# Kernel tuning notes

Measured on AMD Instinct MI355X. Metric: run time of the kernel, lower is better.

Reference implementation:

```python
import jax, jax.numpy as jnp
import numpy as np

N = 50000        # atoms
E = 1600000      # edges (precomputed radius graph)
H = 128          # hidden_channels
F = 64           # num_filters
G = 50           # num_gaussians
L = 3            # num_interactions
NG = 256         # graphs in batch
MAXZ = 100       # atomic-number vocabulary
CUTOFF = 10.0


def ssp(x):
    # ShiftedSoftplus
    return jax.nn.softplus(x) - jnp.log(2.0).astype(x.dtype)


def setup_inputs() -> dict:
    key = jax.random.key(0)
    ks = jax.random.split(key, 20)
    s = 0.1
    inp = {
        "z": jax.random.randint(ks[0], (N,), 0, MAXZ),
        "pos": jax.random.uniform(ks[1], (N, 3), dtype=jnp.float32) * 5.0,
        "batch": jnp.sort(jax.random.randint(ks[2], (N,), 0, NG)),
        "edge_index": jax.random.randint(ks[3], (2, E), 0, N),
        "emb": jax.random.normal(ks[4], (MAXZ, H), dtype=jnp.float32),
        # interaction-block params, stacked over L layers
        "mw1": jax.random.normal(ks[5], (L, G, F), dtype=jnp.float32) * s,
        "mb1": jnp.zeros((L, F), dtype=jnp.float32),
        "mw2": jax.random.normal(ks[6], (L, F, F), dtype=jnp.float32) * s,
        "mb2": jnp.zeros((L, F), dtype=jnp.float32),
        "l1w": jax.random.normal(ks[7], (L, H, F), dtype=jnp.float32) * s,  # no bias
        "l2w": jax.random.normal(ks[8], (L, F, H), dtype=jnp.float32) * s,
        "l2b": jnp.zeros((L, H), dtype=jnp.float32),
        "lw": jax.random.normal(ks[9], (L, H, H), dtype=jnp.float32) * s,
        "lb": jnp.zeros((L, H), dtype=jnp.float32),
        # output MLP
        "ow1": jax.random.normal(ks[10], (H, H // 2), dtype=jnp.float32) * s,
        "ob1": jnp.zeros((H // 2,), dtype=jnp.float32),
        "ow2": jax.random.normal(ks[11], (H // 2, 1), dtype=jnp.float32) * s,
        "ob2": jnp.zeros((1,), dtype=jnp.float32),
    }
    return inp


def reference(z, pos, batch, edge_index, emb, mw1, mb1, mw2, mb2,
              l1w, l2w, l2b, lw, lb, ow1, ob1, ow2, ob2):
    src = edge_index[0]  # j (message source)
    dst = edge_index[1]  # i (message target)

    h = emb[z]                                   # [N,H]

    # edge distances + Gaussian smearing
    d = jnp.linalg.norm(pos[src] - pos[dst], axis=-1)          # [E]
    offset = jnp.linspace(0.0, CUTOFF, G, dtype=jnp.float32)   # [G]
    coeff = -0.5 / (offset[1] - offset[0]) ** 2
    edge_attr = jnp.exp(coeff * (d[:, None] - offset) ** 2)    # [E,G]

    # cosine cutoff
    C = 0.5 * (jnp.cos(d * jnp.pi / CUTOFF) + 1.0)             # [E]

    for i in range(L):
        # per-edge filter MLP
        W = ssp(edge_attr @ mw1[i] + mb1[i]) @ mw2[i] + mb2[i]  # [E,F]
        W = W * C[:, None]
        xj = (h @ l1w[i])[src]                                  # gather [E,F]
        msg = xj * W                                            # [E,F]
        agg = jax.ops.segment_sum(msg, dst, num_segments=N)     # [N,F]
        x = agg @ l2w[i] + l2b[i]                               # [N,H]
        x = ssp(x)
        x = x @ lw[i] + lb[i]
        h = h + x                                               # residual

    # output network + per-graph sum readout
    h = ssp(h @ ow1 + ob1)
    h = h @ ow2 + ob2                                           # [N,1]
    out = jax.ops.segment_sum(h, batch, num_segments=NG)        # [NG,1]
    return out.squeeze(1)                                       # [NG]
```

## Files before the change

kernel.cpp:

```cpp
#include <hip/hip_runtime.h>


typedef short bf16x8 __attribute__((ext_vector_type(8)));
typedef unsigned short ushort8 __attribute__((ext_vector_type(8)));
typedef float floatx4 __attribute__((ext_vector_type(4)));

#define HCH 128
#define FCH 64
#define GCH 50
#define LN  3
#define TBL 4096
#define CAP2 12288
#define CHUNK 4096
#define DMAX 8.6603f

#define MFMA(a, b, c) __builtin_amdgcn_mfma_f32_16x16x32_bf16((a), (b), (c), 0, 0, 0)

__device__ __forceinline__ unsigned short f2bf(float x) {
    unsigned int u = __float_as_uint(x);
    unsigned int r = (u + 0x7FFFu + ((u >> 16) & 1u)) >> 16;
    return (unsigned short)r;
}

__device__ __forceinline__ unsigned pk2bf(float lo, float hi) {
    unsigned ulo = __float_as_uint(lo) + 0x8000u;
    unsigned uhi = __float_as_uint(hi) + 0x8000u;
    return __builtin_amdgcn_perm(uhi, ulo, 0x07060302u);
}

__device__ __forceinline__ float bf2f(unsigned short u) {
    return __uint_as_float((unsigned)u << 16);
}

__device__ __forceinline__ float sspf(float x) {
    float t = __expf(-fabsf(x));
    float l = __logf(1.f + t);
    return fmaxf(x, 0.f) + l - 0.69314718056f;
}

__device__ __forceinline__ void fill_frag(const float* __restrict__ src,
                                          short* __restrict__ dst,
                                          int K, int F, int Ksrc,
                                          int tid, int nthr)
{
    int kc = K >> 5;
    int total = (F >> 4) * kc * 512;
    for (int i = tid; i < total; i += nthr) {
        int j = i & 7;
        int lane = (i >> 3) & 63;
        int rest = i >> 9;
        int kk = rest % kc;
        int nt = rest / kc;
        int k = kk * 32 + ((lane >> 4) << 3) + j;
        int f = nt * 16 + (lane & 15);
        float v = (k < Ksrc) ? src[k * F + f] : 0.f;
        dst[i] = (short)f2bf(v);
    }
}

__global__ void k_prep(const float* __restrict__ l1w, const float* __restrict__ l2w,
                       const float* __restrict__ lw,  const float* __restrict__ ow1,
                       short* __restrict__ l1wp, short* __restrict__ l2wp,
                       short* __restrict__ lwp,  short* __restrict__ ow1p)
{
    int tid = blockIdx.x * blockDim.x + threadIdx.x;
    int nthr = gridDim.x * blockDim.x;
    for (int l = 0; l < LN; l++) {
        fill_frag(l1w + l * HCH * FCH, l1wp + l * 8192, 128, 64, 128, tid, nthr);
        fill_frag(l2w + l * FCH * HCH, l2wp + l * 8192, 64, 128, 64, tid, nthr);
        fill_frag(lw  + l * HCH * HCH, lwp  + l * 16384, 128, 128, 128, tid, nthr);
    }
    fill_frag(ow1, ow1p, 128, 64, 128, tid, nthr);
}

__global__ __launch_bounds__(64) void k_wtab(
    const float* __restrict__ mw1, const float* __restrict__ mb1,
    const float* __restrict__ mw2, const float* __restrict__ mb2,
    unsigned short* __restrict__ Wtb)
{
    __shared__ float sh[64];
    int blk = blockIdx.x;
    int l = blk / TBL, k = blk - l * TBL;
    int f = threadIdx.x;
    float d = (float)k * (DMAX / (float)(TBL - 1));
    const float step = 10.f / 49.f;
    const float coeff = -0.5f / (step * step);

    float t1 = mb1[l * 64 + f];
    const float* w1 = mw1 + l * GCH * 64;
    for (int g = 0; g < GCH; g++) {
        float u = d - (float)g * step;
        t1 += __expf(coeff * u * u) * w1[g * 64 + f];
    }
    sh[f] = sspf(t1);
    float acc = mb2[l * 64 + f];
    const float* w2 = mw2 + l * 64 * 64;
    for (int g = 0; g < 64; g++) acc += sh[g] * w2[g * 64 + f];
    float C = 0.5f * (__cosf(d * 0.31415926535897932f) + 1.f);
    Wtb[(size_t)blk * 64 + f] = f2bf(acc * C);
}

__global__ __launch_bounds__(256) void k_s1(
    const int* __restrict__ ei, const float* __restrict__ pos,
    int* __restrict__ gcur, int2* __restrict__ ebuf, int E, int nb2)
{
    __shared__ int hist[256];
    __shared__ int lstart[256];
    __shared__ int lcur[256];
    __shared__ int gbase[256];
    __shared__ int wsum[4];
    __shared__ int2 stage[CHUNK];

    int t = threadIdx.x, lane = t & 63, w = t >> 6;
    int e0 = blockIdx.x * CHUNK;
    int e1 = min(e0 + CHUNK, E);
    int cnt = e1 - e0;

    hist[t] = 0;
    __syncthreads();

    int2 my[16];
    int  mybk[16];
#pragma unroll
    for (int i = 0; i < 16; i++) {
        int e = e0 + t + i * 256;
        int ec = min(e, E - 1);
        int s = ei[ec];
        int d2 = ei[E + ec];
        float dx = pos[s * 3 + 0] - pos[d2 * 3 + 0];
        float dy = pos[s * 3 + 1] - pos[d2 * 3 + 1];
        float dz = pos[s * 3 + 2] - pos[d2 * 3 + 2];
        float dist = sqrtf(dx * dx + dy * dy + dz * dz);
        int tix = (int)(dist * ((float)(TBL - 1) / DMAX) + 0.5f);
        tix = (tix > TBL - 1) ? (TBL - 1) : tix;
        my[i] = make_int2(s | (tix << 17), d2);
        mybk[i] = (e < e1) ? (d2 >> 8) : -1;
        if (mybk[i] >= 0) atomicAdd(&hist[mybk[i]], 1);
    }
    __syncthreads();

    int base0;
    {
        int c = hist[t];
        int a = c;
#pragma unroll
        for (int o = 1; o < 64; o <<= 1) {
            int u = __shfl_up(a, o, 64);
            if (lane >= o) a += u;
        }
        if (lane == 63) wsum[w] = a;
        __syncthreads();
        int prefix = 0;
#pragma unroll
        for (int i = 0; i < 4; i++) if (i < w) prefix += wsum[i];
        int ls = prefix + a - c;
        lstart[t] = ls; lcur[t] = ls;
        base0 = (c && t < nb2) ? atomicAdd(&gcur[t * 16], c) : 0;
    }
    __syncthreads();

#pragma unroll
    for (int i = 0; i < 16; i++) {
        if (mybk[i] >= 0) {
            int ofs = atomicAdd(&lcur[mybk[i]], 1);
            stage[ofs] = my[i];
        }
    }
    gbase[t] = t * CAP2 + base0;
    __syncthreads();

    for (int i = t; i < cnt; i += 256) {
        int2 ed = stage[i];
        int bk = ed.y >> 8;
        int g = gbase[bk] + (i - lstart[bk]);
        if (g < bk * CAP2 + CAP2) ebuf[g] = ed;
    }
}

__global__ __launch_bounds__(512) void k_s2(
    const int2* __restrict__ ebuf, const int* __restrict__ gcur,
    int2* __restrict__ edata, int* __restrict__ rowptr, int nb2)
{
    __shared__ int hist[256];
    __shared__ int bcur[256];
    __shared__ int wred[8];
    int t = threadIdx.x, lane = t & 63, w = t >> 6, bk = blockIdx.x;
    int cnt = min(gcur[bk * 16], CAP2);

    int v = (t < bk && t < nb2) ? min(gcur[t * 16], CAP2) : 0;
#pragma unroll
    for (int o = 32; o; o >>= 1) v += __shfl_down(v, o, 64);
    if (lane == 0) wred[w] = v;
    if (t < 256) hist[t] = 0;
    __syncthreads();
    int gs = 0;
#pragma unroll
    for (int i = 0; i < 8; i++) gs += wred[i];

    const int2* eb = ebuf + (size_t)bk * CAP2;
    for (int i = t; i < cnt; i += 512)
        atomicAdd(&hist[eb[i].y & 255], 1);
    __syncthreads();
    int myc = (t < 256) ? hist[t] : 0;
    for (int o = 1; o < 256; o <<= 1) {
        int u = (t < 256 && t >= o) ? hist[t - o] : 0;
        __syncthreads();
        if (t < 256) hist[t] += u;
        __syncthreads();
    }
    if (t < 256) {
        int start = gs + hist[t] - myc;
        bcur[t] = start;
        rowptr[(bk << 8) + t] = start;
    }
    if (bk == nb2 - 1 && t == 0) rowptr[nb2 << 8] = gs + cnt;
    __syncthreads();
    for (int i = t; i < cnt; i += 512) {
        int2 ed = eb[i];
        int dl = ed.y & 255;
        int p = atomicAdd(&bcur[dl], 1);
        edata[p] = ed;
    }
}

__global__ __launch_bounds__(256) void k_node0(const int* __restrict__ z,
    const float* __restrict__ emb, const short* __restrict__ l1wp0,
    float* __restrict__ h, unsigned short* __restrict__ xjb, int N)
{
    __shared__ __align__(16) short A3[8192];
    __shared__ int zL[64];
    int t = threadIdx.x, lane = t & 63, w = t >> 6;
    int n0 = blockIdx.x * 64;
    if (t < 64) { int n = n0 + t; zL[t] = (n < N) ? z[n] : 0; }
    __syncthreads();
#pragma unroll
    for (int m = 0; m < 16; m++) {
        int ii = lane + 64 * m;
        int rloc = ii >> 6;
        int k0 = (ii & 63) * 2;
        int n = n0 + w * 16 + rloc;
        float2 v = make_float2(0.f, 0.f);
        if (n < N) {
            v = *(const float2*)(&emb[(size_t)zL[w * 16 + rloc] * HCH + k0]);
            *(float2*)(&h[(size_t)n * HCH + k0]) = v;
        }
        unsigned pk = pk2bf(v.x, v.y);
        int si = w * 2048 + (k0 >> 5) * 512 + (rloc + 16 * ((k0 >> 3) & 3)) * 8 + (k0 & 7);
        *(unsigned*)(&A3[si]) = pk;
    }
    int quad = lane >> 4, col = lane & 15;
    const bf16x8* B = (const bf16x8*)l1wp0;
    bf16x8 af[4];
#pragma unroll
    for (int kk = 0; kk < 4; kk++)
        af[kk] = *(const bf16x8*)(&A3[w * 2048 + kk * 512 + lane * 8]);
#pragma unroll
    for (int nt = 0; nt < 4; nt++) {
        floatx4 c = {0.f, 0.f, 0.f, 0.f};
#pragma unroll
        for (int kk = 0; kk < 4; kk++) c = MFMA(af[kk], B[(nt * 4 + kk) * 64 + lane], c);
        int f = nt * 16 + col;
#pragma unroll
        for (int reg = 0; reg < 4; reg++) {
            int n = n0 + w * 16 + quad * 4 + reg;
            if (n < N) xjb[(size_t)n * FCH + f] = f2bf(c[reg]);
        }
    }
}

__global__ __launch_bounds__(256) void k_edge(
    const int* __restrict__ rowptr, const int2* __restrict__ edata,
    const unsigned short* __restrict__ xjb, const unsigned short* __restrict__ Wt,
    unsigned short* __restrict__ aggb, int N)
{
    int t = threadIdx.x, lane = t & 63, w = t >> 6;
    int n = blockIdx.x * 4 + w;
    if (n >= N) return;
    int beg = rowptr[n];
    int end = rowptr[n + 1];
    int slot = lane >> 3;
    int cq = (lane & 7) * 8;
    const unsigned short* xp = xjb + cq;
    const unsigned short* wp = Wt + cq;
    float acc[8];
#pragma unroll
    for (int j = 0; j < 8; j++) acc[j] = 0.f;
    for (int e = beg; e < end; e += 16) {
        int eb = e + slot * 2;
        int2 ed0 = edata[min(eb + 0, end - 1)];
        int2 ed1 = edata[min(eb + 1, end - 1)];
        int exv[2] = {ed0.x, ed1.x};
        uint4 xq[2], wq[2];
#pragma unroll
        for (int i = 0; i < 2; i++) {
            int s   = exv[i] & 0x1FFFF;
            int tix = (int)(((unsigned)exv[i]) >> 17);
            xq[i] = *(const uint4*)(xp + ((size_t)s << 6));
            wq[i] = *(const uint4*)(wp + ((size_t)tix << 6));
        }
#pragma unroll
        for (int i = 0; i < 2; i++) {
            if (eb + i >= end) { wq[i].x = 0u; wq[i].y = 0u; wq[i].z = 0u; wq[i].w = 0u; }
            acc[0] += __uint_as_float(xq[i].x << 16)         * __uint_as_float(wq[i].x << 16);
            acc[1] += __uint_as_float(xq[i].x & 0xFFFF0000u) * __uint_as_float(wq[i].x & 0xFFFF0000u);
            acc[2] += __uint_as_float(xq[i].y << 16)         * __uint_as_float(wq[i].y << 16);
            acc[3] += __uint_as_float(xq[i].y & 0xFFFF0000u) * __uint_as_float(wq[i].y & 0xFFFF0000u);
            acc[4] += __uint_as_float(xq[i].z << 16)         * __uint_as_float(wq[i].z << 16);
            acc[5] += __uint_as_float(xq[i].z & 0xFFFF0000u) * __uint_as_float(wq[i].z & 0xFFFF0000u);
            acc[6] += __uint_as_float(xq[i].w << 16)         * __uint_as_float(wq[i].w << 16);
            acc[7] += __uint_as_float(xq[i].w & 0xFFFF0000u) * __uint_as_float(wq[i].w & 0xFFFF0000u);
        }
    }
#pragma unroll
    for (int o = 8; o < 64; o <<= 1) {
#pragma unroll
        for (int j = 0; j < 8; j++) acc[j] += __shfl_xor(acc[j], o, 64);
    }
    if (slot == 0) {
        uint4 pk;
        pk.x = pk2bf(acc[0], acc[1]);
        pk.y = pk2bf(acc[2], acc[3]);
        pk.z = pk2bf(acc[4], acc[5]);
        pk.w = pk2bf(acc[6], acc[7]);
        *(uint4*)(aggb + (size_t)n * FCH + cq) = pk;
    }
}

__global__ __launch_bounds__(256) void k_update(
    const unsigned short* __restrict__ aggb, const short* __restrict__ l2wp,
    const float* __restrict__ l2b, const short* __restrict__ lwp,
    const float* __restrict__ lb,  const short* __restrict__ l1wp_next,
    float* __restrict__ h, unsigned short* __restrict__ xjb, int layer, int N)
{
    __shared__ __align__(16) short AR[8192];
    int t = threadIdx.x, lane = t & 63, w = t >> 6;
    int n0 = blockIdx.x * 64;
    short* WR = &AR[w * 2048];
#pragma unroll
    for (int m = 0; m < 8; m++) {
        int ii = lane + 64 * m;
        int rloc = ii >> 5;
        int k0 = (ii & 31) * 2;
        int n = n0 + w * 16 + rloc;
        unsigned pk = 0u;
        if (n < N) pk = *(const unsigned*)(&aggb[(size_t)n * FCH + k0]);
        int si = (k0 >> 5) * 512 + (rloc + 16 * ((k0 >> 3) & 3)) * 8 + (k0 & 7);
        *(unsigned*)(&WR[si]) = pk;
    }
    int quad = lane >> 4, col = lane & 15;
    const bf16x8* Bl2 = (const bf16x8*)(l2wp + layer * 8192);
    const bf16x8* Blw = (const bf16x8*)(lwp + layer * 16384);
    const bf16x8* Bl1 = (const bf16x8*)l1wp_next;

    bf16x8 a0 = *(const bf16x8*)(&WR[lane * 8]);
    bf16x8 a1 = *(const bf16x8*)(&WR[512 + lane * 8]);
#pragma unroll
    for (int nt = 0; nt < 8; nt++) {
        float bias = l2b[layer * HCH + nt * 16 + col];
        floatx4 c = {bias, bias, bias, bias};
        c = MFMA(a0, Bl2[(nt * 2 + 0) * 64 + lane], c);
        c = MFMA(a1, Bl2[(nt * 2 + 1) * 64 + lane], c);
        int f = nt * 16 + col;
        int si0 = (f >> 5) * 512 + (16 * ((f >> 3) & 3)) * 8 + (f & 7);
#pragma unroll
        for (int reg = 0; reg < 4; reg++)
            WR[si0 + (quad * 4 + reg) * 8] = (short)f2bf(sspf(c[reg]));
    }
    bf16x8 af[4];
#pragma unroll
    for (int kk = 0; kk < 4; kk++)
        af[kk] = *(const bf16x8*)(&WR[kk * 512 + lane * 8]);
#pragma unroll
    for (int nt = 0; nt < 8; nt++) {
        float bias = lb[layer * HCH + nt * 16 + col];
        floatx4 c = {bias, bias, bias, bias};
#pragma unroll
        for (int kk = 0; kk < 4; kk++) c = MFMA(af[kk], Blw[(nt * 4 + kk) * 64 + lane], c);
        int f = nt * 16 + col;
        int si0 = (f >> 5) * 512 + (16 * ((f >> 3) & 3)) * 8 + (f & 7);
#pragma unroll
        for (int reg = 0; reg < 4; reg++) {
            int n = n0 + w * 16 + quad * 4 + reg;
            float hv = 0.f;
            if (n < N) {
                hv = h[(size_t)n * HCH + f] + c[reg];
                h[(size_t)n * HCH + f] = hv;
            }
            WR[si0 + (quad * 4 + reg) * 8] = (short)f2bf(hv);
        }
    }
#pragma unroll
    for (int kk = 0; kk < 4; kk++)
        af[kk] = *(const bf16x8*)(&WR[kk * 512 + lane * 8]);
#pragma unroll
    for (int nt = 0; nt < 4; nt++) {
        floatx4 c = {0.f, 0.f, 0.f, 0.f};
#pragma unroll
        for (int kk = 0; kk < 4; kk++) c = MFMA(af[kk], Bl1[(nt * 4 + kk) * 64 + lane], c);
        int f = nt * 16 + col;
#pragma unroll
        for (int reg = 0; reg < 4; reg++) {
            int n = n0 + w * 16 + quad * 4 + reg;
            if (n < N) xjb[(size_t)n * FCH + f] = f2bf(c[reg]);
        }
    }
}

__global__ __launch_bounds__(256) void k_final(
    const unsigned short* __restrict__ aggb, const short* __restrict__ l2wp,
    const float* __restrict__ l2b, const short* __restrict__ lwp,
    const float* __restrict__ lb,  const short* __restrict__ ow1p,
    const float* __restrict__ ob1, const float* __restrict__ ow2,
    const float* __restrict__ ob2, const int* __restrict__ batch,
    const float* __restrict__ h, float* __restrict__ out, int layer, int N)
{
    __shared__ __align__(16) short AR[8192];
    __shared__ float R[64 * 17];
    int t = threadIdx.x, lane = t & 63, w = t >> 6;
    int n0 = blockIdx.x * 64;
    short* WR = &AR[w * 2048];
#pragma unroll
    for (int m = 0; m < 8; m++) {
        int ii = lane + 64 * m;
        int rloc = ii >> 5;
        int k0 = (ii & 31) * 2;
        int n = n0 + w * 16 + rloc;
        unsigned pk = 0u;
        if (n < N) pk = *(const unsigned*)(&aggb[(size_t)n * FCH + k0]);
        int si = (k0 >> 5) * 512 + (rloc + 16 * ((k0 >> 3) & 3)) * 8 + (k0 & 7);
        *(unsigned*)(&WR[si]) = pk;
    }
    int quad = lane >> 4, col = lane & 15;
    const bf16x8* Bl2 = (const bf16x8*)(l2wp + layer * 8192);
    const bf16x8* Blw = (const bf16x8*)(lwp + layer * 16384);
    const bf16x8* Bow = (const bf16x8*)ow1p;

    bf16x8 a0 = *(const bf16x8*)(&WR[lane * 8]);
    bf16x8 a1 = *(const bf16x8*)(&WR[512 + lane * 8]);
#pragma unroll
    for (int nt = 0; nt < 8; nt++) {
        float bias = l2b[layer * HCH + nt * 16 + col];
        floatx4 c = {bias, bias, bias, bias};
        c = MFMA(a0, Bl2[(nt * 2 + 0) * 64 + lane], c);
        c = MFMA(a1, Bl2[(nt * 2 + 1) * 64 + lane], c);
        int f = nt * 16 + col;
        int si0 = (f >> 5) * 512 + (16 * ((f >> 3) & 3)) * 8 + (f & 7);
#pragma unroll
        for (int reg = 0; reg < 4; reg++)
            WR[si0 + (quad * 4 + reg) * 8] = (short)f2bf(sspf(c[reg]));
    }
    bf16x8 af[4];
#pragma unroll
    for (int kk = 0; kk < 4; kk++)
        af[kk] = *(const bf16x8*)(&WR[kk * 512 + lane * 8]);
#pragma unroll
    for (int nt = 0; nt < 8; nt++) {
        float bias = lb[layer * HCH + nt * 16 + col];
        floatx4 c = {bias, bias, bias, bias};
#pragma unroll
        for (int kk = 0; kk < 4; kk++) c = MFMA(af[kk], Blw[(nt * 4 + kk) * 64 + lane], c);
        int f = nt * 16 + col;
        int si0 = (f >> 5) * 512 + (16 * ((f >> 3) & 3)) * 8 + (f & 7);
#pragma unroll
        for (int reg = 0; reg < 4; reg++) {
            int n = n0 + w * 16 + quad * 4 + reg;
            float hv = 0.f;
            if (n < N) hv = h[(size_t)n * HCH + f] + c[reg];
            WR[si0 + (quad * 4 + reg) * 8] = (short)f2bf(hv);
        }
    }
#pragma unroll
    for (int kk = 0; kk < 4; kk++)
        af[kk] = *(const bf16x8*)(&WR[kk * 512 + lane * 8]);
    float p[4] = {0.f, 0.f, 0.f, 0.f};
#pragma unroll
    for (int nt = 0; nt < 4; nt++) {
        float bias = ob1[nt * 16 + col];
        floatx4 c = {bias, bias, bias, bias};
#pragma unroll
        for (int kk = 0; kk < 4; kk++) c = MFMA(af[kk], Bow[(nt * 4 + kk) * 64 + lane], c);
        float w2 = ow2[nt * 16 + col];
#pragma unroll
        for (int reg = 0; reg < 4; reg++) p[reg] += sspf(c[reg]) * w2;
    }
#pragma unroll
    for (int reg = 0; reg < 4; reg++)
        R[(w * 16 + quad * 4 + reg) * 17 + col] = p[reg];
    __syncthreads();
    if (t < 64) {
        int n = n0 + t;
        float v = 0.f;
        int g = -1;
        if (n < N) {
            v = ob2[0];
#pragma unroll
            for (int c2 = 0; c2 < 16; c2++) v += R[t * 17 + c2];
            g = batch[n];
        }
#pragma unroll
        for (int off2 = 1; off2 < 64; off2 <<= 1) {
            float vv = __shfl_down(v, off2, 64);
            int gg = __shfl_down(g, off2, 64);
            if (lane + off2 < 64 && gg == g) v += vv;
        }
        int gp = __shfl_up(g, 1, 64);
        bool head = (lane == 0) || (g != gp);
        if (head && g >= 0) unsafeAtomicAdd(&out[g], v);
    }
}

extern "C" void kernel_launch(void* const* d_in, const int* in_sizes, int n_in,
                              void* d_out, int out_size, void* d_ws, size_t ws_size,
                              hipStream_t stream)
{
    const int*   z    = (const int*)d_in[0];
    const float* pos  = (const float*)d_in[1];
    const int*   batc = (const int*)d_in[2];
    const int*   ei   = (const int*)d_in[3];
    const float* emb  = (const float*)d_in[4];
    const float* mw1  = (const float*)d_in[5];
    const float* mb1  = (const float*)d_in[6];
    const float* mw2  = (const float*)d_in[7];
    const float* mb2  = (const float*)d_in[8];
    const float* l1w  = (const float*)d_in[9];
    const float* l2w  = (const float*)d_in[10];
    const float* l2b  = (const float*)d_in[11];
    const float* lw   = (const float*)d_in[12];
    const float* lb   = (const float*)d_in[13];
    const float* ow1  = (const float*)d_in[14];
    const float* ob1  = (const float*)d_in[15];
    const float* ow2  = (const float*)d_in[16];
    const float* ob2  = (const float*)d_in[17];
    float* out = (float*)d_out;

    int N = in_sizes[0];
    int E = in_sizes[3] / 2;
    int nb2 = (N + 255) >> 8;

    char* ws = (char*)d_ws;
    size_t off = 0;
    auto alloc = [&](size_t bytes) {
        void* p = ws + off;
        off = (off + bytes + 255) & ~(size_t)255;
        return p;
    };
    float* h      = (float*)alloc((size_t)N * HCH * 4);
    unsigned short* xjb = (unsigned short*)alloc((size_t)N * FCH * 2);
    unsigned short* aggb = (unsigned short*)alloc((size_t)N * FCH * 2);
    int2*  ebuf   = (int2*)alloc((size_t)nb2 * CAP2 * 8);
    int2*  edata  = (int2*)alloc((size_t)E * 8);
    unsigned short* Wtab = (unsigned short*)alloc((size_t)LN * TBL * 64 * 2);
    int*   gcur   = (int*)alloc((size_t)nb2 * 64);
    int*   rowptr = (int*)alloc(((size_t)nb2 * 256 + 1) * 4);
    short* l1wp   = (short*)alloc(LN * 8192 * 2);
    short* l2wp   = (short*)alloc(LN * 8192 * 2);
    short* lwp    = (short*)alloc(LN * 16384 * 2);
    short* ow1p   = (short*)alloc(8192 * 2);

    int NB = (N + 63) / 64;
    int NB4 = (N + 3) / 4;
    int S1B = (E + CHUNK - 1) / CHUNK;

    k_prep<<<32, 256, 0, stream>>>(l1w, l2w, lw, ow1, l1wp, l2wp, lwp, ow1p);
    k_wtab<<<LN * TBL, 64, 0, stream>>>(mw1, mb1, mw2, mb2, Wtab);
    hipMemsetAsync(gcur, 0, (size_t)nb2 * 64, stream);
    k_s1<<<S1B, 256, 0, stream>>>(ei, pos, gcur, ebuf, E, nb2);
    k_s2<<<nb2, 512, 0, stream>>>(ebuf, gcur, edata, rowptr, nb2);
    hipMemsetAsync(out, 0, (size_t)out_size * sizeof(float), stream);

    k_node0<<<NB, 256, 0, stream>>>(z, emb, l1wp, h, xjb, N);
    for (int l = 0; l < LN; l++) {
        k_edge<<<NB4, 256, 0, stream>>>(rowptr, edata, xjb,
                                        Wtab + (size_t)l * TBL * 64, aggb, N);
        if (l < LN - 1) {
            k_update<<<NB, 256, 0, stream>>>(aggb, l2wp, l2b, lwp, lb,
                                             l1wp + (l + 1) * 8192, h, xjb, l, N);
        } else {
            k_final<<<NB, 256, 0, stream>>>(aggb, l2wp, l2b, lwp, lb, ow1p,
                                            ob1, ow2, ob2, batc, h, out, l, N);
        }
    }
}
```

Baseline: 335.6 us.

## Fuse edge aggregation into node update kernels and merge setup launches

```diff
diff --git a/kernel.cpp b/kernel.cpp
--- a/kernel.cpp
+++ b/kernel.cpp
@@ -58,46 +58,49 @@
     }
 }
 
-__global__ void k_prep(const float* __restrict__ l1w, const float* __restrict__ l2w,
-                       const float* __restrict__ lw,  const float* __restrict__ ow1,
-                       short* __restrict__ l1wp, short* __restrict__ l2wp,
-                       short* __restrict__ lwp,  short* __restrict__ ow1p)
-{
-    int tid = blockIdx.x * blockDim.x + threadIdx.x;
-    int nthr = gridDim.x * blockDim.x;
-    for (int l = 0; l < LN; l++) {
-        fill_frag(l1w + l * HCH * FCH, l1wp + l * 8192, 128, 64, 128, tid, nthr);
-        fill_frag(l2w + l * FCH * HCH, l2wp + l * 8192, 64, 128, 64, tid, nthr);
-        fill_frag(lw  + l * HCH * HCH, lwp  + l * 16384, 128, 128, 128, tid, nthr);
-    }
-    fill_frag(ow1, ow1p, 128, 64, 128, tid, nthr);
-}
-
-__global__ __launch_bounds__(64) void k_wtab(
+__global__ __launch_bounds__(64) void k_pre(
     const float* __restrict__ mw1, const float* __restrict__ mb1,
     const float* __restrict__ mw2, const float* __restrict__ mb2,
-    unsigned short* __restrict__ Wtb)
+    unsigned short* __restrict__ Wtb,
+    const float* __restrict__ l1w, const float* __restrict__ l2w,
+    const float* __restrict__ lw,  const float* __restrict__ ow1,
+    short* __restrict__ l1wp, short* __restrict__ l2wp,
+    short* __restrict__ lwp,  short* __restrict__ ow1p,
+    int* __restrict__ gcur, float* __restrict__ out, int nb2, int osz)
 {
     __shared__ float sh[64];
     int blk = blockIdx.x;
-    int l = blk / TBL, k = blk - l * TBL;
     int f = threadIdx.x;
-    float d = (float)k * (DMAX / (float)(TBL - 1));
-    const float step = 10.f / 49.f;
-    const float coeff = -0.5f / (step * step);
-
-    float t1 = mb1[l * 64 + f];
-    const float* w1 = mw1 + l * GCH * 64;
-    for (int g = 0; g < GCH; g++) {
-        float u = d - (float)g * step;
-        t1 += __expf(coeff * u * u) * w1[g * 64 + f];
-    }
-    sh[f] = sspf(t1);
-    float acc = mb2[l * 64 + f];
-    const float* w2 = mw2 + l * 64 * 64;
-    for (int g = 0; g < 64; g++) acc += sh[g] * w2[g * 64 + f];
-    float C = 0.5f * (__cosf(d * 0.31415926535897932f) + 1.f);
-    Wtb[(size_t)blk * 64 + f] = f2bf(acc * C);
+    if (blk < LN * TBL) {
+        int l = blk / TBL, k = blk - l * TBL;
+        float d = (float)k * (DMAX / (float)(TBL - 1));
+        const float step = 10.f / 49.f;
+        const float coeff = -0.5f / (step * step);
+        float t1 = mb1[l * 64 + f];
+        const float* w1 = mw1 + l * GCH * 64;
+        for (int g = 0; g < GCH; g++) {
+            float u = d - (float)g * step;
+            t1 += __expf(coeff * u * u) * w1[g * 64 + f];
+        }
+        sh[f] = sspf(t1);
+        float acc = mb2[l * 64 + f];
+        const float* w2 = mw2 + l * 64 * 64;
+        for (int g = 0; g < 64; g++) acc += sh[g] * w2[g * 64 + f];
+        float C = 0.5f * (__cosf(d * 0.31415926535897932f) + 1.f);
+        Wtb[(size_t)blk * 64 + f] = f2bf(acc * C);
+    } else if (blk < LN * TBL + 32) {
+        int tid = (blk - LN * TBL) * 64 + f;
+        int nthr = 32 * 64;
+        for (int l = 0; l < LN; l++) {
+            fill_frag(l1w + l * HCH * FCH, l1wp + l * 8192, 128, 64, 128, tid, nthr);
+            fill_frag(l2w + l * FCH * HCH, l2wp + l * 8192, 64, 128, 64, tid, nthr);
+            fill_frag(lw  + l * HCH * HCH, lwp  + l * 16384, 128, 128, 128, tid, nthr);
+        }
+        fill_frag(ow1, ow1p, 128, 64, 128, tid, nthr);
+    } else {
+        for (int i = f; i < nb2 * 16; i += 64) gcur[i] = 0;
+        for (int i = f; i < osz; i += 64) out[i] = 0.f;
+    }
 }
 
 __global__ __launch_bounds__(256) void k_s1(
@@ -177,176 +180,171 @@
     }
 }
 
-__global__ __launch_bounds__(512) void k_s2(
+__global__ __launch_bounds__(512) void k_s2n0(
     const int2* __restrict__ ebuf, const int* __restrict__ gcur,
-    int2* __restrict__ edata, int* __restrict__ rowptr, int nb2)
+    int2* __restrict__ edata, int* __restrict__ rowptr, int nb2,
+    const int* __restrict__ z, const float* __restrict__ emb,
+    const short* __restrict__ l1wp0, float* __restrict__ h,
+    unsigned short* __restrict__ xjb, int N)
 {
     __shared__ int hist[256];
     __shared__ int bcur[256];
     __shared__ int wred[8];
-    int t = threadIdx.x, lane = t & 63, w = t >> 6, bk = blockIdx.x;
-    int cnt = min(gcur[bk * 16], CAP2);
-
-    int v = (t < bk && t < nb2) ? min(gcur[t * 16], CAP2) : 0;
-#pragma unroll
-    for (int o = 32; o; o >>= 1) v += __shfl_down(v, o, 64);
-    if (lane == 0) wred[w] = v;
-    if (t < 256) hist[t] = 0;
-    __syncthreads();
-    int gs = 0;
-#pragma unroll
-    for (int i = 0; i < 8; i++) gs += wred[i];
-
-    const int2* eb = ebuf + (size_t)bk * CAP2;
-    for (int i = t; i < cnt; i += 512)
-        atomicAdd(&hist[eb[i].y & 255], 1);
-    __syncthreads();
-    int myc = (t < 256) ? hist[t] : 0;
-    for (int o = 1; o < 256; o <<= 1) {
-        int u = (t < 256 && t >= o) ? hist[t - o] : 0;
-        __syncthreads();
-        if (t < 256) hist[t] += u;
-        __syncthreads();
-    }
-    if (t < 256) {
-        int start = gs + hist[t] - myc;
-        bcur[t] = start;
-        rowptr[(bk << 8) + t] = start;
-    }
-    if (bk == nb2 - 1 && t == 0) rowptr[nb2 << 8] = gs + cnt;
-    __syncthreads();
-    for (int i = t; i < cnt; i += 512) {
-        int2 ed = eb[i];
-        int dl = ed.y & 255;
-        int p = atomicAdd(&bcur[dl], 1);
-        edata[p] = ed;
-    }
-}
-
-__global__ __launch_bounds__(256) void k_node0(const int* __restrict__ z,
-    const float* __restrict__ emb, const short* __restrict__ l1wp0,
-    float* __restrict__ h, unsigned short* __restrict__ xjb, int N)
-{
     __shared__ __align__(16) short A3[8192];
     __shared__ int zL[64];
     int t = threadIdx.x, lane = t & 63, w = t >> 6;
-    int n0 = blockIdx.x * 64;
-    if (t < 64) { int n = n0 + t; zL[t] = (n < N) ? z[n] : 0; }
-    __syncthreads();
-#pragma unroll
-    for (int m = 0; m < 16; m++) {
-        int ii = lane + 64 * m;
-        int rloc = ii >> 6;
-        int k0 = (ii & 63) * 2;
-        int n = n0 + w * 16 + rloc;
-        float2 v = make_float2(0.f, 0.f);
-        if (n < N) {
-            v = *(const float2*)(&emb[(size_t)zL[w * 16 + rloc] * HCH + k0]);
-            *(float2*)(&h[(size_t)n * HCH + k0]) = v;
-        }
-        unsigned pk = pk2bf(v.x, v.y);
-        int si = w * 2048 + (k0 >> 5) * 512 + (rloc + 16 * ((k0 >> 3) & 3)) * 8 + (k0 & 7);
-        *(unsigned*)(&A3[si]) = pk;
-    }
-    int quad = lane >> 4, col = lane & 15;
-    const bf16x8* B = (const bf16x8*)l1wp0;
-    bf16x8 af[4];
-#pragma unroll
-    for (int kk = 0; kk < 4; kk++)
-        af[kk] = *(const bf16x8*)(&A3[w * 2048 + kk * 512 + lane * 8]);
-#pragma unroll
-    for (int nt = 0; nt < 4; nt++) {
-        floatx4 c = {0.f, 0.f, 0.f, 0.f};
-#pragma unroll
-        for (int kk = 0; kk < 4; kk++) c = MFMA(af[kk], B[(nt * 4 + kk) * 64 + lane], c);
-        int f = nt * 16 + col;
-#pragma unroll
-        for (int reg = 0; reg < 4; reg++) {
-            int n = n0 + w * 16 + quad * 4 + reg;
-            if (n < N) xjb[(size_t)n * FCH + f] = f2bf(c[reg]);
-        }
-    }
-}
-
-__global__ __launch_bounds__(256) void k_edge(
+    int bk = blockIdx.x;
+    if (bk < nb2) {
+        int cnt = min(gcur[bk * 16], CAP2);
+        int v = (t < bk && t < nb2) ? min(gcur[t * 16], CAP2) : 0;
+#pragma unroll
+        for (int o = 32; o; o >>= 1) v += __shfl_down(v, o, 64);
+        if (lane == 0) wred[w] = v;
+        if (t < 256) hist[t] = 0;
+        __syncthreads();
+        int gs = 0;
+#pragma unroll
+        for (int i = 0; i < 8; i++) gs += wred[i];
+
+        const int2* eb = ebuf + (size_t)bk * CAP2;
+        for (int i = t; i < cnt; i += 512)
+            atomicAdd(&hist[eb[i].y & 255], 1);
+        __syncthreads();
+        int myc = (t < 256) ? hist[t] : 0;
+        for (int o = 1; o < 256; o <<= 1) {
+            int u = (t < 256 && t >= o) ? hist[t - o] : 0;
+            __syncthreads();
+            if (t < 256) hist[t] += u;
+            __syncthreads();
+        }
+        if (t < 256) {
+            int start = gs + hist[t] - myc;
+            bcur[t] = start;
+            rowptr[(bk << 8) + t] = start;
+        }
+        if (bk == nb2 - 1 && t == 0) rowptr[nb2 << 8] = gs + cnt;
+        __syncthreads();
+        for (int i = t; i < cnt; i += 512) {
+            int2 ed = eb[i];
+            int dl = ed.y & 255;
+            int p = atomicAdd(&bcur[dl], 1);
+            edata[p] = ed;
+        }
+    } else {
+        int n0 = (bk - nb2) * 64;
+        if (t < 64) { int n = n0 + t; zL[t] = (n < N) ? z[n] : 0; }
+        __syncthreads();
+        if (t < 256) {
+#pragma unroll
+            for (int m = 0; m < 16; m++) {
+                int ii = lane + 64 * m;
+                int rloc = ii >> 6;
+                int k0 = (ii & 63) * 2;
+                int n = n0 + w * 16 + rloc;
+                float2 v = make_float2(0.f, 0.f);
+                if (n < N) {
+                    v = *(const float2*)(&emb[(size_t)zL[w * 16 + rloc] * HCH + k0]);
+                    *(float2*)(&h[(size_t)n * HCH + k0]) = v;
+                }
+                unsigned pk = pk2bf(v.x, v.y);
+                int si = w * 2048 + (k0 >> 5) * 512 + (rloc + 16 * ((k0 >> 3) & 3)) * 8 + (k0 & 7);
+                *(unsigned*)(&A3[si]) = pk;
+            }
+            int quad = lane >> 4, col = lane & 15;
+            const bf16x8* B = (const bf16x8*)l1wp0;
+            bf16x8 af[4];
+#pragma unroll
+            for (int kk = 0; kk < 4; kk++)
+                af[kk] = *(const bf16x8*)(&A3[w * 2048 + kk * 512 + lane * 8]);
+#pragma unroll
+            for (int nt = 0; nt < 4; nt++) {
+                floatx4 c = {0.f, 0.f, 0.f, 0.f};
+#pragma unroll
+                for (int kk = 0; kk < 4; kk++) c = MFMA(af[kk], B[(nt * 4 + kk) * 64 + lane], c);
+                int f = nt * 16 + col;
+#pragma unroll
+                for (int reg = 0; reg < 4; reg++) {
+                    int n = n0 + w * 16 + quad * 4 + reg;
+                    if (n < N) xjb[(size_t)n * FCH + f] = f2bf(c[reg]);
+                }
+            }
+        }
+    }
+}
+
+__device__ __forceinline__ void edge_phase(
     const int* __restrict__ rowptr, const int2* __restrict__ edata,
-    const unsigned short* __restrict__ xjb, const unsigned short* __restrict__ Wt,
-    unsigned short* __restrict__ aggb, int N)
-{
-    int t = threadIdx.x, lane = t & 63, w = t >> 6;
-    int n = blockIdx.x * 4 + w;
-    if (n >= N) return;
-    int beg = rowptr[n];
-    int end = rowptr[n + 1];
+    const unsigned short* __restrict__ xin, const unsigned short* __restrict__ Wt,
+    short* __restrict__ WR, int nbase, int lane)
+{
     int slot = lane >> 3;
     int cq = (lane & 7) * 8;
-    const unsigned short* xp = xjb + cq;
+    const unsigned short* xp = xin + cq;
     const unsigned short* wp = Wt + cq;
-    float acc[8];
-#pragma unroll
-    for (int j = 0; j < 8; j++) acc[j] = 0.f;
-    for (int e = beg; e < end; e += 16) {
-        int eb = e + slot * 2;
-        int2 ed0 = edata[min(eb + 0, end - 1)];
-        int2 ed1 = edata[min(eb + 1, end - 1)];
-        int exv[2] = {ed0.x, ed1.x};
-        uint4 xq[2], wq[2];
-#pragma unroll
-        for (int i = 0; i < 2; i++) {
-            int s   = exv[i] & 0x1FFFF;
-            int tix = (int)(((unsigned)exv[i]) >> 17);
-            xq[i] = *(const uint4*)(xp + ((size_t)s << 6));
-            wq[i] = *(const uint4*)(wp + ((size_t)tix << 6));
-        }
-#pragma unroll
-        for (int i = 0; i < 2; i++) {
-            if (eb + i >= end) { wq[i].x = 0u; wq[i].y = 0u; wq[i].z = 0u; wq[i].w = 0u; }
-            acc[0] += __uint_as_float(xq[i].x << 16)         * __uint_as_float(wq[i].x << 16);
-            acc[1] += __uint_as_float(xq[i].x & 0xFFFF0000u) * __uint_as_float(wq[i].x & 0xFFFF0000u);
-            acc[2] += __uint_as_float(xq[i].y << 16)         * __uint_as_float(wq[i].y << 16);
-            acc[3] += __uint_as_float(xq[i].y & 0xFFFF0000u) * __uint_as_float(wq[i].y & 0xFFFF0000u);
-            acc[4] += __uint_as_float(xq[i].z << 16)         * __uint_as_float(wq[i].z << 16);
-            acc[5] += __uint_as_float(xq[i].z & 0xFFFF0000u) * __uint_as_float(wq[i].z & 0xFFFF0000u);
-            acc[6] += __uint_as_float(xq[i].w << 16)         * __uint_as_float(wq[i].w << 16);
-            acc[7] += __uint_as_float(xq[i].w & 0xFFFF0000u) * __uint_as_float(wq[i].w & 0xFFFF0000u);
-        }
-    }
-#pragma unroll
-    for (int o = 8; o < 64; o <<= 1) {
-#pragma unroll
-        for (int j = 0; j < 8; j++) acc[j] += __shfl_xor(acc[j], o, 64);
-    }
-    if (slot == 0) {
-        uint4 pk;
-        pk.x = pk2bf(acc[0], acc[1]);
-        pk.y = pk2bf(acc[2], acc[3]);
-        pk.z = pk2bf(acc[4], acc[5]);
-        pk.w = pk2bf(acc[6], acc[7]);
-        *(uint4*)(aggb + (size_t)n * FCH + cq) = pk;
-    }
-}
-
-__global__ __launch_bounds__(256) void k_update(
-    const unsigned short* __restrict__ aggb, const short* __restrict__ l2wp,
-    const float* __restrict__ l2b, const short* __restrict__ lwp,
-    const float* __restrict__ lb,  const short* __restrict__ l1wp_next,
-    float* __restrict__ h, unsigned short* __restrict__ xjb, int layer, int N)
+    int rp = (lane < 17) ? rowptr[nbase + lane] : 0;
+    for (int i = 0; i < 16; i++) {
+        int beg = __shfl(rp, i, 64);
+        int end = __shfl(rp, i + 1, 64);
+        float acc[8];
+#pragma unroll
+        for (int j = 0; j < 8; j++) acc[j] = 0.f;
+        for (int e = beg; e < end; e += 16) {
+            int eb = e + slot * 2;
+            int2 ed0 = edata[min(eb + 0, end - 1)];
+            int2 ed1 = edata[min(eb + 1, end - 1)];
+            int exv[2] = {ed0.x, ed1.x};
+            uint4 xq[2], wq[2];
+#pragma unroll
+            for (int k = 0; k < 2; k++) {
+                int s   = exv[k] & 0x1FFFF;
+                int tix = (int)(((unsigned)exv[k]) >> 17);
+                xq[k] = *(const uint4*)(xp + ((size_t)s << 6));
+                wq[k] = *(const uint4*)(wp + ((size_t)tix << 6));
+            }
+#pragma unroll
+            for (int k = 0; k < 2; k++) {
+                if (eb + k >= end) { wq[k].x = 0u; wq[k].y = 0u; wq[k].z = 0u; wq[k].w = 0u; }
+                acc[0] += __uint_as_float(xq[k].x << 16)         * __uint_as_float(wq[k].x << 16);
+                acc[1] += __uint_as_float(xq[k].x & 0xFFFF0000u) * __uint_as_float(wq[k].x & 0xFFFF0000u);
+                acc[2] += __uint_as_float(xq[k].y << 16)         * __uint_as_float(wq[k].y << 16);
+                acc[3] += __uint_as_float(xq[k].y & 0xFFFF0000u) * __uint_as_float(wq[k].y & 0xFFFF0000u);
+                acc[4] += __uint_as_float(xq[k].z << 16)         * __uint_as_float(wq[k].z << 16);
+                acc[5] += __uint_as_float(xq[k].z & 0xFFFF0000u) * __uint_as_float(wq[k].z & 0xFFFF0000u);
+                acc[6] += __uint_as_float(xq[k].w << 16)         * __uint_as_float(wq[k].w << 16);
+                acc[7] += __uint_as_float(xq[k].w & 0xFFFF0000u) * __uint_as_float(wq[k].w & 0xFFFF0000u);
+            }
+        }
+#pragma unroll
+        for (int o = 8; o < 64; o <<= 1) {
+#pragma unroll
+            for (int j = 0; j < 8; j++) acc[j] += __shfl_xor(acc[j], o, 64);
+        }
+        if (slot == 0) {
+#pragma unroll
+            for (int j = 0; j < 4; j++) {
+                int k0 = cq + 2 * j;
+                int si = (k0 >> 5) * 512 + (i + 16 * ((k0 >> 3) & 3)) * 8 + (k0 & 7);
+                *(unsigned*)(&WR[si]) = pk2bf(acc[2 * j], acc[2 * j + 1]);
+            }
+        }
+    }
+}
+
+__global__ __launch_bounds__(256) void k_eu(
+    const int* __restrict__ rowptr, const int2* __restrict__ edata,
+    const unsigned short* __restrict__ xin, const unsigned short* __restrict__ Wt,
+    const short* __restrict__ l2wp, const float* __restrict__ l2b,
+    const short* __restrict__ lwp,  const float* __restrict__ lb,
+    const short* __restrict__ l1wp_next,
+    float* __restrict__ h, unsigned short* __restrict__ xout, int layer, int N)
 {
     __shared__ __align__(16) short AR[8192];
     int t = threadIdx.x, lane = t & 63, w = t >> 6;
     int n0 = blockIdx.x * 64;
     short* WR = &AR[w * 2048];
-#pragma unroll
-    for (int m = 0; m < 8; m++) {
-        int ii = lane + 64 * m;
-        int rloc = ii >> 5;
-        int k0 = (ii & 31) * 2;
-        int n = n0 + w * 16 + rloc;
-        unsigned pk = 0u;
-        if (n < N) pk = *(const unsigned*)(&aggb[(size_t)n * FCH + k0]);
-        int si = (k0 >> 5) * 512 + (rloc + 16 * ((k0 >> 3) & 3)) * 8 + (k0 & 7);
-        *(unsigned*)(&WR[si]) = pk;
-    }
+
+    edge_phase(rowptr, edata, xin, Wt, WR, n0 + w * 16, lane);
+
     int quad = lane >> 4, col = lane & 15;
     const bf16x8* Bl2 = (const bf16x8*)(l2wp + layer * 8192);
     const bf16x8* Blw = (const bf16x8*)(lwp + layer * 16384);
@@ -401,35 +399,29 @@
 #pragma unroll
         for (int reg = 0; reg < 4; reg++) {
             int n = n0 + w * 16 + quad * 4 + reg;
-            if (n < N) xjb[(size_t)n * FCH + f] = f2bf(c[reg]);
-        }
-    }
-}
-
-__global__ __launch_bounds__(256) void k_final(
-    const unsigned short* __restrict__ aggb, const short* __restrict__ l2wp,
-    const float* __restrict__ l2b, const short* __restrict__ lwp,
-    const float* __restrict__ lb,  const short* __restrict__ ow1p,
-    const float* __restrict__ ob1, const float* __restrict__ ow2,
-    const float* __restrict__ ob2, const int* __restrict__ batch,
-    const float* __restrict__ h, float* __restrict__ out, int layer, int N)
+            if (n < N) xout[(size_t)n * FCH + f] = f2bf(c[reg]);
+        }
+    }
+}
+
+__global__ __launch_bounds__(256) void k_ef(
+    const int* __restrict__ rowptr, const int2* __restrict__ edata,
+    const unsigned short* __restrict__ xin, const unsigned short* __restrict__ Wt,
+    const short* __restrict__ l2wp, const float* __restrict__ l2b,
+    const short* __restrict__ lwp,  const float* __restrict__ lb,
+    const short* __restrict__ ow1p, const float* __restrict__ ob1,
+    const float* __restrict__ ow2,  const float* __restrict__ ob2,
+    const int* __restrict__ batch,  const float* __restrict__ h,
+    float* __restrict__ out, int layer, int N)
 {
     __shared__ __align__(16) short AR[8192];
     __shared__ float R[64 * 17];
     int t = threadIdx.x, lane = t & 63, w = t >> 6;
     int n0 = blockIdx.x * 64;
     short* WR = &AR[w * 2048];
-#pragma unroll
-    for (int m = 0; m < 8; m++) {
-        int ii = lane + 64 * m;
-        int rloc = ii >> 5;
-        int k0 = (ii & 31) * 2;
-        int n = n0 + w * 16 + rloc;
-        unsigned pk = 0u;
-        if (n < N) pk = *(const unsigned*)(&aggb[(size_t)n * FCH + k0]);
-        int si = (k0 >> 5) * 512 + (rloc + 16 * ((k0 >> 3) & 3)) * 8 + (k0 & 7);
-        *(unsigned*)(&WR[si]) = pk;
-    }
+
+    edge_phase(rowptr, edata, xin, Wt, WR, n0 + w * 16, lane);
+
     int quad = lane >> 4, col = lane & 15;
     const bf16x8* Bl2 = (const bf16x8*)(l2wp + layer * 8192);
     const bf16x8* Blw = (const bf16x8*)(lwp + layer * 16384);
@@ -545,8 +537,8 @@
         return p;
     };
     float* h      = (float*)alloc((size_t)N * HCH * 4);
-    unsigned short* xjb = (unsigned short*)alloc((size_t)N * FCH * 2);
-    unsigned short* aggb = (unsigned short*)alloc((size_t)N * FCH * 2);
+    unsigned short* xjb0 = (unsigned short*)alloc((size_t)N * FCH * 2);
+    unsigned short* xjb1 = (unsigned short*)alloc((size_t)N * FCH * 2);
     int2*  ebuf   = (int2*)alloc((size_t)nb2 * CAP2 * 8);
     int2*  edata  = (int2*)alloc((size_t)E * 8);
     unsigned short* Wtab = (unsigned short*)alloc((size_t)LN * TBL * 64 * 2);
@@ -558,26 +550,22 @@
     short* ow1p   = (short*)alloc(8192 * 2);
 
     int NB = (N + 63) / 64;
-    int NB4 = (N + 3) / 4;
     int S1B = (E + CHUNK - 1) / CHUNK;
-
-    k_prep<<<32, 256, 0, stream>>>(l1w, l2w, lw, ow1, l1wp, l2wp, lwp, ow1p);
-    k_wtab<<<LN * TBL, 64, 0, stream>>>(mw1, mb1, mw2, mb2, Wtab);
-    hipMemsetAsync(gcur, 0, (size_t)nb2 * 64, stream);
+    int PREB = LN * TBL + 32 + 1;
+
+    k_pre<<<PREB, 64, 0, stream>>>(mw1, mb1, mw2, mb2, Wtab,
+                                   l1w, l2w, lw, ow1, l1wp, l2wp, lwp, ow1p,
+                                   gcur, out, nb2, out_size);
     k_s1<<<S1B, 256, 0, stream>>>(ei, pos, gcur, ebuf, E, nb2);
-    k_s2<<<nb2, 512, 0, stream>>>(ebuf, gcur, edata, rowptr, nb2);
-    hipMemsetAsync(out, 0, (size_t)out_size * sizeof(float), stream);
-
-    k_node0<<<NB, 256, 0, stream>>>(z, emb, l1wp, h, xjb, N);
-    for (int l = 0; l < LN; l++) {
-        k_edge<<<NB4, 256, 0, stream>>>(rowptr, edata, xjb,
-                                        Wtab + (size_t)l * TBL * 64, aggb, N);
-        if (l < LN - 1) {
-            k_update<<<NB, 256, 0, stream>>>(aggb, l2wp, l2b, lwp, lb,
-                                             l1wp + (l + 1) * 8192, h, xjb, l, N);
-        } else {
-            k_final<<<NB, 256, 0, stream>>>(aggb, l2wp, l2b, lwp, lb, ow1p,
-                                            ob1, ow2, ob2, batc, h, out, l, N);
-        }
-    }
-}
+    k_s2n0<<<nb2 + NB, 512, 0, stream>>>(ebuf, gcur, edata, rowptr, nb2,
+                                         z, emb, l1wp, h, xjb0, N);
+    k_eu<<<NB, 256, 0, stream>>>(rowptr, edata, xjb0, Wtab,
+                                 l2wp, l2b, lwp, lb, l1wp + 8192,
+                                 h, xjb1, 0, N);
+    k_eu<<<NB, 256, 0, stream>>>(rowptr, edata, xjb1, Wtab + (size_t)TBL * 64,
+                                 l2wp, l2b, lwp, lb, l1wp + 2 * 8192,
+                                 h, xjb0, 1, N);
+    k_ef<<<NB, 256, 0, stream>>>(rowptr, edata, xjb0, Wtab + (size_t)2 * TBL * 64,
+                                 l2wp, l2b, lwp, lb, ow1p, ob1, ow2, ob2,
+                                 batc, h, out, 2, N);
+}
```

New measurement: 353.3 us. 1.05x slower.
